# Performance work log

Hardware: AMD Instinct MI355X
Metric: run time of the kernel (lower is better)

Reference implementation:

```python
import jax, jax.numpy as jnp
import numpy as np

B, L, C, H = 8, 1024, 1024, 16  # batch, seq_len, n_embed, n_head


def setup_inputs() -> dict:
    key = jax.random.key(0)
    k0, k1, k2 = jax.random.split(key, 3)
    s = 0.02  # init scale
    return {
        "x": jax.random.normal(k0, (B, L, C), jnp.float32),
        "W_qkv": jax.random.normal(k1, (C, 3 * C), jnp.float32) * s,  # (in, out) layout
        "b_qkv": jnp.zeros((3 * C,), jnp.float32),
        "W_proj": jax.random.normal(k2, (C, C), jnp.float32) * s,
        "b_proj": jnp.zeros((C,), jnp.float32),
    }


def reference(x, W_qkv, b_qkv, W_proj, b_proj):
    Bb, Ll, Cc = x.shape
    d = Cc // H  # head dim
    qkv = x @ W_qkv + b_qkv                      # (B, L, 3C)
    q, k, v = jnp.split(qkv, 3, axis=2)
    q = q.reshape(Bb, Ll, H, d).transpose(0, 2, 1, 3)  # (B, H, L, d)
    k = k.reshape(Bb, Ll, H, d).transpose(0, 2, 1, 3)
    v = v.reshape(Bb, Ll, H, d).transpose(0, 2, 1, 3)
    scale = 1.0 / np.sqrt(d).astype(np.float32)
    attn = jnp.einsum("bhid,bhjd->bhij", q, k) * scale  # (B, H, Lq, Lk)
    causal = jnp.tril(jnp.ones((Ll, Ll), dtype=bool))    # (Lq, Lk)
    attn = jnp.where(causal[None, None, :, :], attn, -jnp.inf)
    # NOTE: source uses F.softmax(attn, dim=2) -> softmax over the QUERY axis.
    attn = jax.nn.softmax(attn, axis=2)
    y = jnp.einsum("bhij,bhjd->bhid", attn, v)           # (B, H, L, d)
    y = y.transpose(0, 2, 1, 3).reshape(Bb, Ll, Cc)      # (B, L, C)
    return y @ W_proj + b_proj
```

## Files before the change

kernel.cpp:

```cpp
#include <hip/hip_runtime.h>

typedef unsigned short u16;
typedef unsigned int   u32;
using bf16x8 = __attribute__((ext_vector_type(8))) short;
using f32x4  = __attribute__((ext_vector_type(4))) float;
using f32x16 = __attribute__((ext_vector_type(16))) float;
using u32x4  = __attribute__((ext_vector_type(4))) u32;

static constexpr int Bb = 8, Ll = 1024, Cc = 1024, Hh = 16, Dd = 64;
static constexpr int Mrows = Bb * Ll;
static constexpr int N3    = 3 * Cc;
static constexpr float QSCALE = 0.125f * 1.44269504088896f;

__device__ __forceinline__ u16 f2b(float f) {
    u32 u = __builtin_bit_cast(u32, f);
    u += 0x7FFFu + ((u >> 16) & 1u);
    return (u16)(u >> 16);
}
__device__ __forceinline__ float b2f(u16 u) {
    return __builtin_bit_cast(float, (u32)u << 16);
}
__device__ __forceinline__ u32 pack2bf(float a, float b) {
    return (u32)f2b(a) | ((u32)f2b(b) << 16);
}
__device__ __forceinline__ void gload16(const u16* g, u16* l) {
    __builtin_amdgcn_global_load_lds(
        (const __attribute__((address_space(1))) void*)g,
        (__attribute__((address_space(3))) void*)l, 16, 0, 0);
}

__global__ void k_prep(const float* __restrict__ x, u16* __restrict__ xb,
                       const float* __restrict__ Wqkv, u16* __restrict__ WqkvT,
                       const float* __restrict__ Wproj, u16* __restrict__ WprojT)
{
    __shared__ float tile[32][33];
    int bid = blockIdx.x;
    int tid = threadIdx.x;
    if (bid < 2048) {
        int idx = bid * 256 + tid;
        #pragma unroll
        for (int h = 0; h < 2; ++h) {
            f32x4 v0 = *((const f32x4*)x + idx * 4 + h * 2);
            f32x4 v1 = *((const f32x4*)x + idx * 4 + h * 2 + 1);
            u32x4 o;
            o[0] = pack2bf(v0[0], v0[1]);
            o[1] = pack2bf(v0[2], v0[3]);
            o[2] = pack2bf(v1[0], v1[1]);
            o[3] = pack2bf(v1[2], v1[3]);
            *((u32x4*)xb + idx * 2 + h) = o;
        }
        return;
    }
    int bz = bid - 2048;
    int bx = bz & 127;
    int by = bz >> 7;
    const float* in; u16* out; int Cn;
    if (bx < 96) { in = Wqkv;  out = WqkvT;  Cn = N3; }
    else         { in = Wproj; out = WprojT; Cn = Cc; bx -= 96; }
    const int R = Cc;
    int tx = tid & 31, ty = tid >> 5;
    int c = bx * 32 + tx;
    int rbase = by * 32;
    #pragma unroll
    for (int rr = 0; rr < 4; ++rr)
        tile[ty + rr * 8][tx] = in[(size_t)(rbase + ty + rr * 8) * Cn + c];
    __syncthreads();
    int ro = bx * 32 + ty;
    #pragma unroll
    for (int rr = 0; rr < 4; ++rr)
        out[(size_t)(ro + rr * 8) * R + rbase + tx] = f2b(tile[tx][ty + rr * 8]);
}

__global__ __launch_bounds__(256, 2)
void k_gemm_qkv32(const u16* __restrict__ A, const u16* __restrict__ Bt,
                  const float* __restrict__ bias,
                  u16* __restrict__ qo, u16* __restrict__ ko, u16* __restrict__ vo)
{
    const int K = Cc;
    const int NT = K / 64;
    __shared__ u16 As[2][128 * 64];
    __shared__ u16 Bs[2][128 * 64];
    const int tid = threadIdx.x;
    const int wid = tid >> 6, lane = tid & 63;
    const int l31 = lane & 31, lhi = lane >> 5, l7 = lane & 7;
    const int wr = wid >> 1, wc = wid & 1;
    const int nwg = gridDim.x * gridDim.y;
    const int flat = blockIdx.y * gridDim.x + blockIdx.x;
    const int swz = (flat & 7) * (nwg >> 3) + (flat >> 3);
    const int bx = swz % gridDim.x, by = swz / gridDim.x;
    const int row0 = by * 128, col0 = bx * 128;

    const int srow = tid >> 3;
    const int schunk = (tid & 7) ^ (srow & 7);
    const u16* gA = A  + (size_t)(row0 + srow) * K + schunk * 8;
    const u16* gB = Bt + (size_t)(col0 + srow) * K + schunk * 8;

#define STG(buf, t) do { \
    const u16* ga_ = gA + (size_t)(t) * 64; \
    const u16* gb_ = gB + (size_t)(t) * 64; \
    u16* la_ = &As[buf][wid * 512]; \
    u16* lb_ = &Bs[buf][wid * 512]; \
    gload16(ga_,                  la_); \
    gload16(ga_ + (size_t)32 * K, la_ + 2048); \
    gload16(ga_ + (size_t)64 * K, la_ + 4096); \
    gload16(ga_ + (size_t)96 * K, la_ + 6144); \
    gload16(gb_,                  lb_); \
    gload16(gb_ + (size_t)32 * K, lb_ + 2048); \
    gload16(gb_ + (size_t)64 * K, lb_ + 4096); \
    gload16(gb_ + (size_t)96 * K, lb_ + 6144); \
} while (0)

    const int coff0 = (((0 + lhi) ^ l7) << 3);
    const int coff1 = (((2 + lhi) ^ l7) << 3);
    const int coff2 = (((4 + lhi) ^ l7) << 3);
    const int coff3 = (((6 + lhi) ^ l7) << 3);
    const int coff[4] = { coff0, coff1, coff2, coff3 };

    f32x16 acc[2][2] = {};

    STG(0, 0);
    STG(1, 1);
    asm volatile("s_waitcnt vmcnt(8)" ::: "memory");
    __builtin_amdgcn_s_barrier();
    __builtin_amdgcn_sched_barrier(0);

    for (int t = 0; t < NT; ++t) {
        const u16* cA = &As[t & 1][0];
        const u16* cB = &Bs[t & 1][0];
        bf16x8 af[2][4], bf0[4];
        #pragma unroll
        for (int tm = 0; tm < 2; ++tm)
            #pragma unroll
            for (int kc = 0; kc < 4; ++kc)
                af[tm][kc] = *(const bf16x8*)&cA[(wr * 64 + tm * 32 + l31) * 64 + coff[kc]];
        #pragma unroll
        for (int kc = 0; kc < 4; ++kc)
            bf0[kc] = *(const bf16x8*)&cB[(wc * 64 + l31) * 64 + coff[kc]];
        __builtin_amdgcn_s_setprio(1);
        #pragma unroll
        for (int tm = 0; tm < 2; ++tm)
            #pragma unroll
            for (int kc = 0; kc < 4; ++kc)
                acc[tm][0] = __builtin_amdgcn_mfma_f32_32x32x16_bf16(
                    af[tm][kc], bf0[kc], acc[tm][0], 0, 0, 0);
        __builtin_amdgcn_s_setprio(0);
        __builtin_amdgcn_s_barrier();
        bf16x8 bf1[4];
        #pragma unroll
        for (int kc = 0; kc < 4; ++kc)
            bf1[kc] = *(const bf16x8*)&cB[(wc * 64 + 32 + l31) * 64 + coff[kc]];
        __builtin_amdgcn_s_setprio(1);
        #pragma unroll
        for (int tm = 0; tm < 2; ++tm)
            #pragma unroll
            for (int kc = 0; kc < 4; ++kc)
                acc[tm][1] = __builtin_amdgcn_mfma_f32_32x32x16_bf16(
                    af[tm][kc], bf1[kc], acc[tm][1], 0, 0, 0);
        __builtin_amdgcn_s_setprio(0);
        __builtin_amdgcn_s_barrier();
        __builtin_amdgcn_sched_barrier(0);
        if (t + 2 < NT) STG(t & 1, t + 2);
        if (t + 1 < NT) {
            if (t + 2 < NT) { asm volatile("s_waitcnt vmcnt(8)" ::: "memory"); }
            else            { asm volatile("s_waitcnt vmcnt(0)" ::: "memory"); }
            __builtin_amdgcn_s_barrier();
            __builtin_amdgcn_sched_barrier(0);
        }
    }
#undef STG

    #pragma unroll
    for (int tm = 0; tm < 2; ++tm) {
        #pragma unroll
        for (int tn = 0; tn < 2; ++tn) {
            int cg = col0 + wc * 64 + tn * 32 + l31;
            float bv = bias[cg];
            int which = cg >> 10;
            float sc = (which == 0) ? QSCALE : 1.0f;
            int cc2 = cg & 1023;
            int h = cc2 >> 6, dd = cc2 & 63;
            int rbase = row0 + wr * 64 + tm * 32 + 4 * lhi;
            #pragma unroll
            for (int g = 0; g < 4; ++g) {
                #pragma unroll
                for (int r = 0; r < 4; ++r) {
                    int rg = rbase + 8 * g + r;
                    int bidx = rg >> 10, ll2 = rg & 1023;
                    size_t o = ((size_t)(bidx * Hh + h) * Ll + ll2) * Dd + dd;
                    u16 val = f2b((acc[tm][tn][g * 4 + r] + bv) * sc);
                    if (which == 0) qo[o] = val;
                    else if (which == 1) ko[o] = val;
                    else vo[o] = val;
                }
            }
        }
    }
}

__global__ __launch_bounds__(256, 2)
void k_gemm_proj32(const u16* __restrict__ A, const u16* __restrict__ Bt,
                   const float* __restrict__ bias, float* __restrict__ outf)
{
    const int K = Cc;
    const int N = Cc;
    const int NT = K / 64;
    __shared__ u16 As[2][128 * 64];
    __shared__ u16 Bs[2][128 * 64];
    const int tid = threadIdx.x;
    const int wid = tid >> 6, lane = tid & 63;
    const int l31 = lane & 31, lhi = lane >> 5, l7 = lane & 7;
    const int wr = wid >> 1, wc = wid & 1;
    const int nwg = gridDim.x * gridDim.y;
    const int flat = blockIdx.y * gridDim.x + blockIdx.x;
    const int swz = (flat & 7) * (nwg >> 3) + (flat >> 3);
    const int bx = swz % gridDim.x, by = swz / gridDim.x;
    const int row0 = by * 128, col0 = bx * 128;

    const int srow = tid >> 3;
    const int schunk = (tid & 7) ^ (srow & 7);
    const u16* gA = A  + (size_t)(row0 + srow) * K + schunk * 8;
    const u16* gB = Bt + (size_t)(col0 + srow) * K + schunk * 8;

#define STG(buf, t) do { \
    const u16* ga_ = gA + (size_t)(t) * 64; \
    const u16* gb_ = gB + (size_t)(t) * 64; \
    u16* la_ = &As[buf][wid * 512]; \
    u16* lb_ = &Bs[buf][wid * 512]; \
    gload16(ga_,                  la_); \
    gload16(ga_ + (size_t)32 * K, la_ + 2048); \
    gload16(ga_ + (size_t)64 * K, la_ + 4096); \
    gload16(ga_ + (size_t)96 * K, la_ + 6144); \
    gload16(gb_,                  lb_); \
    gload16(gb_ + (size_t)32 * K, lb_ + 2048); \
    gload16(gb_ + (size_t)64 * K, lb_ + 4096); \
    gload16(gb_ + (size_t)96 * K, lb_ + 6144); \
} while (0)

    const int coff0 = (((0 + lhi) ^ l7) << 3);
    const int coff1 = (((2 + lhi) ^ l7) << 3);
    const int coff2 = (((4 + lhi) ^ l7) << 3);
    const int coff3 = (((6 + lhi) ^ l7) << 3);
    const int coff[4] = { coff0, coff1, coff2, coff3 };

    f32x16 acc[2][2] = {};

    STG(0, 0);
    STG(1, 1);
    asm volatile("s_waitcnt vmcnt(8)" ::: "memory");
    __builtin_amdgcn_s_barrier();
    __builtin_amdgcn_sched_barrier(0);

    for (int t = 0; t < NT; ++t) {
        const u16* cA = &As[t & 1][0];
        const u16* cB = &Bs[t & 1][0];
        bf16x8 af[2][4], bf0[4];
        #pragma unroll
        for (int tm = 0; tm < 2; ++tm)
            #pragma unroll
            for (int kc = 0; kc < 4; ++kc)
                af[tm][kc] = *(const bf16x8*)&cA[(wr * 64 + tm * 32 + l31) * 64 + coff[kc]];
        #pragma unroll
        for (int kc = 0; kc < 4; ++kc)
            bf0[kc] = *(const bf16x8*)&cB[(wc * 64 + l31) * 64 + coff[kc]];
        __builtin_amdgcn_s_setprio(1);
        #pragma unroll
        for (int tm = 0; tm < 2; ++tm)
            #pragma unroll
            for (int kc = 0; kc < 4; ++kc)
                acc[tm][0] = __builtin_amdgcn_mfma_f32_32x32x16_bf16(
                    af[tm][kc], bf0[kc], acc[tm][0], 0, 0, 0);
        __builtin_amdgcn_s_setprio(0);
        __builtin_amdgcn_s_barrier();
        bf16x8 bf1[4];
        #pragma unroll
        for (int kc = 0; kc < 4; ++kc)
            bf1[kc] = *(const bf16x8*)&cB[(wc * 64 + 32 + l31) * 64 + coff[kc]];
        __builtin_amdgcn_s_setprio(1);
        #pragma unroll
        for (int tm = 0; tm < 2; ++tm)
            #pragma unroll
            for (int kc = 0; kc < 4; ++kc)
                acc[tm][1] = __builtin_amdgcn_mfma_f32_32x32x16_bf16(
                    af[tm][kc], bf1[kc], acc[tm][1], 0, 0, 0);
        __builtin_amdgcn_s_setprio(0);
        __builtin_amdgcn_s_barrier();
        __builtin_amdgcn_sched_barrier(0);
        if (t + 2 < NT) STG(t & 1, t + 2);
        if (t + 1 < NT) {
            if (t + 2 < NT) { asm volatile("s_waitcnt vmcnt(8)" ::: "memory"); }
            else            { asm volatile("s_waitcnt vmcnt(0)" ::: "memory"); }
            __builtin_amdgcn_s_barrier();
            __builtin_amdgcn_sched_barrier(0);
        }
    }
#undef STG

    #pragma unroll
    for (int tm = 0; tm < 2; ++tm) {
        #pragma unroll
        for (int tn = 0; tn < 2; ++tn) {
            int cg = col0 + wc * 64 + tn * 32 + l31;
            float bv = bias[cg];
            int rbase = row0 + wr * 64 + tm * 32 + 4 * lhi;
            #pragma unroll
            for (int g = 0; g < 4; ++g) {
                #pragma unroll
                for (int r = 0; r < 4; ++r) {
                    int rg = rbase + 8 * g + r;
                    outf[(size_t)rg * N + cg] = acc[tm][tn][g * 4 + r] + bv;
                }
            }
        }
    }
}

__global__ __launch_bounds__(256, 4)
void k_attn_colsum_vt(const u16* __restrict__ Q, const u16* __restrict__ Kb,
                      const u16* __restrict__ V, u16* __restrict__ vt)
{
    __shared__ u16 Qs[2][64 * 64];
    __shared__ float zlds[2][64];
    const int tid = threadIdx.x;
    const int wid = tid >> 6, lane = tid & 63;
    const int lr = lane & 15, lg = lane >> 4;
    const int l7 = lr & 7;
    const int fid = blockIdx.x;
    const int xcd = fid & 7, n = fid >> 3;
    const int xtA = n & 7;
    const int xtB = 15 - xtA;
    const int bh = (xcd << 4) | (n >> 3);
    const u16* Qp = Q  + (size_t)bh * Ll * Dd;
    const u16* Kp = Kb + (size_t)bh * Ll * Dd;
    const int jwA = xtA * 64 + wid * 16;
    const int jwB = xtB * 64 + wid * 16;
    bf16x8 kbA0 = *(const bf16x8*)&Kp[(jwA + lr) * Dd + lg * 8];
    bf16x8 kbA1 = *(const bf16x8*)&Kp[(jwA + lr) * Dd + 32 + lg * 8];
    bf16x8 kbB0 = *(const bf16x8*)&Kp[(jwB + lr) * Dd + lg * 8];
    bf16x8 kbB1 = *(const bf16x8*)&Kp[(jwB + lr) * Dd + 32 + lg * 8];
    const bool dmask[4] = { lg * 4 + 0 >= lr, lg * 4 + 1 >= lr,
                            lg * 4 + 2 >= lr, lg * 4 + 3 >= lr };
    const int ch0 = ((lg ^ l7) << 3);
    const int ch1 = (((4 + lg) ^ l7) << 3);
    const int srow = tid >> 3;
    const int schunk = (tid & 7) ^ (srow & 7);
    float zA = 0.f, zB = 0.f;

    const int nA = 16 - xtA;
    const int NS = 17;
#define IOF(s) (((s) < nA) ? (xtA * 64 + 64 * (s)) : (xtB * 64 + 64 * ((s) - nA)))

#define STGQ(buf, I0) do { \
    const u16* g_ = Qp + (size_t)((I0) + srow) * 64 + schunk * 8; \
    u16* l_ = &Qs[buf][wid * 512]; \
    gload16(g_,                   l_); \
    gload16(g_ + (size_t)32 * 64, l_ + 2048); \
} while (0)

#define CS_STEP(buf, I0, JW, KB0, KB1, ZACC) do { \
    const u16* Qs_ = &Qs[buf][0]; \
    _Pragma("unroll") \
    for (int ss = 0; ss < 4; ++ss) { \
        int ib = (I0) + ss * 16; \
        if (ib >= (JW)) { \
            bf16x8 qa0 = *(const bf16x8*)&Qs_[(ss * 16 + lr) * 64 + ch0]; \
            bf16x8 qa1 = *(const bf16x8*)&Qs_[(ss * 16 + lr) * 64 + ch1]; \
            f32x4 s_ = {0.f, 0.f, 0.f, 0.f}; \
            s_ = __builtin_amdgcn_mfma_f32_16x16x32_bf16(qa0, KB0, s_, 0, 0, 0); \
            s_ = __builtin_amdgcn_mfma_f32_16x16x32_bf16(qa1, KB1, s_, 0, 0, 0); \
            if (ib >= (JW) + 16) { \
                _Pragma("unroll") \
                for (int r = 0; r < 4; ++r) ZACC += exp2f(s_[r]); \
            } else { \
                _Pragma("unroll") \
                for (int r = 0; r < 4; ++r) ZACC += dmask[r] ? exp2f(s_[r]) : 0.f; \
            } \
        } \
    } \
} while (0)

    STGQ(0, IOF(0));
    STGQ(1, IOF(1));
    asm volatile("s_waitcnt vmcnt(2)" ::: "memory");
    __builtin_amdgcn_s_barrier();
    __builtin_amdgcn_sched_barrier(0);

    for (int s = 0; s < NS; ++s) {
        if (s < nA) { CS_STEP((s & 1), xtA * 64 + 64 * s, jwA, kbA0, kbA1, zA); }
        else        { CS_STEP((s & 1), xtB * 64 + 64 * (s - nA), jwB, kbB0, kbB1, zB); }
        __builtin_amdgcn_s_barrier();
        __builtin_amdgcn_sched_barrier(0);
        if (s + 2 < NS) STGQ((s & 1), IOF(s + 2));
        if (s + 1 < NS) {
            if (s + 2 < NS) { asm volatile("s_waitcnt vmcnt(2)" ::: "memory"); }
            else            { asm volatile("s_waitcnt vmcnt(0)" ::: "memory"); }
            __builtin_amdgcn_s_barrier();
            __builtin_amdgcn_sched_barrier(0);
        }
    }
#undef STGQ
#undef CS_STEP
#undef IOF

    zA += __shfl_xor(zA, 16); zA += __shfl_xor(zA, 32);
    zB += __shfl_xor(zB, 16); zB += __shfl_xor(zB, 32);
    if (lg == 0) {
        zlds[0][wid * 16 + lr] = 1.f / zA;
        zlds[1][wid * 16 + lr] = 1.f / zB;
    }

    u16* sc = &Qs[0][0];
    const u16* Vr = V + (size_t)bh * Ll * Dd;
    const int lrow = tid >> 2;
    const int seg  = (tid & 3) << 4;
    #pragma unroll
    for (int t = 0; t < 2; ++t) {
        const int jw0 = (t ? xtB : xtA) * 64;
        u32x4 h0 = *(const u32x4*)&Vr[(size_t)(jw0 + lrow) * Dd + seg];
        u32x4 h1 = *(const u32x4*)&Vr[(size_t)(jw0 + lrow) * Dd + seg + 8];
        __syncthreads();
        *(u32x4*)&sc[lrow * 72 + seg]     = h0;
        *(u32x4*)&sc[lrow * 72 + seg + 8] = h1;
        __syncthreads();
        u16 obuf[16];
        #pragma unroll
        for (int j = 0; j < 16; ++j) {
            float zv = zlds[t][seg + j];
            obuf[j] = f2b(b2f(sc[(seg + j) * 72 + lrow]) * zv);
        }
        u16* dst = vt + ((size_t)bh * Dd + lrow) * Ll + jw0 + seg;
        *(u32x4*)dst       = *(u32x4*)&obuf[0];
        *(u32x4*)(dst + 8) = *(u32x4*)&obuf[8];
    }
}

__global__ __launch_bounds__(256, 4)
void k_attn_pv(const u16* __restrict__ Q, const u16* __restrict__ Kb,
               const u16* __restrict__ Vt, u16* __restrict__ Y)
{
    __shared__ u16 Ks[2][64 * 64];
    __shared__ u16 Vs[2][64 * 64];
    const int tid = threadIdx.x;
    const int wid = tid >> 6, lane = tid & 63;
    const int lr = lane & 15, lg = lane >> 4;
    const int l7 = lr & 7;
    const int fid = blockIdx.x;
    const int xcd = fid & 7, n = fid >> 3;
    const int xtA = n & 7;
    const int xtB = 15 - xtA;
    const int bh = (xcd << 4) | (n >> 3);
    const int bidx = bh >> 4, h = bh & 15;
    const u16* Qp = Q  + (size_t)bh * Ll * Dd;
    const u16* Kp = Kb + (size_t)bh * Ll * Dd;
    const u16* Vp = Vt + (size_t)bh * Ll * Dd;
    const int src0 = lr + 32 * (lg & 1);
    const int src1 = src0 + 16;
    const bool selHi = (lg & 2) != 0;
    const int ch0 = ((lg ^ l7) << 3);
    const int ch1 = (((4 + lg) ^ l7) << 3);
    const int srow = tid >> 3;
    const int schunk = (tid & 7) ^ (srow & 7);

    const int iwA = xtA * 64 + wid * 16;
    const int iwB = xtB * 64 + wid * 16;
    bf16x8 qaA0 = *(const bf16x8*)&Qp[(iwA + lr) * Dd + lg * 8];
    bf16x8 qaA1 = *(const bf16x8*)&Qp[(iwA + lr) * Dd + 32 + lg * 8];
    bf16x8 qaB0 = *(const bf16x8*)&Qp[(iwB + lr) * Dd + lg * 8];
    bf16x8 qaB1 = *(const bf16x8*)&Qp[(iwB + lr) * Dd + 32 + lg * 8];
    f32x4 yaccA[4] = {};
    f32x4 yaccB[4] = {};

    const int NS = 17;
#define JOF(s) (((s) <= xtA) ? 64 * (s) : 64 * ((s) - xtA - 1))

#define STGKV(buf, J) do { \
    const u16* gk_ = Kp + (size_t)((J) + srow) * 64 + schunk * 8; \
    const u16* gv_ = Vp + (size_t)srow * Ll + (J) + schunk * 8; \
    u16* lk_ = &Ks[buf][wid * 512]; \
    u16* lv_ = &Vs[buf][wid * 512]; \
    gload16(gk_,                   lk_); \
    gload16(gk_ + (size_t)32 * 64, lk_ + 2048); \
    gload16(gv_,                   lv_); \
    gload16(gv_ + (size_t)32 * Ll, lv_ + 2048); \
} while (0)

#define PV_STEP(buf, J0, IW, QA0, QA1, YACC) do { \
    const u16* Ks_ = &Ks[buf][0]; \
    const u16* Vs_ = &Vs[buf][0]; \
    uint2 w0, w1, w2, w3; \
    _Pragma("unroll") \
    for (int cs = 0; cs < 4; ++cs) { \
        bf16x8 kb0 = *(const bf16x8*)&Ks_[(cs * 16 + lr) * 64 + ch0]; \
        bf16x8 kb1 = *(const bf16x8*)&Ks_[(cs * 16 + lr) * 64 + ch1]; \
        f32x4 s_ = {0.f, 0.f, 0.f, 0.f}; \
        s_ = __builtin_amdgcn_mfma_f32_16x16x32_bf16(kb0, QA0, s_, 0, 0, 0); \
        s_ = __builtin_amdgcn_mfma_f32_16x16x32_bf16(kb1, QA1, s_, 0, 0, 0); \
        int jb = (J0) + cs * 16; \
        float p[4]; \
        if (jb + 15 <= (IW)) { \
            _Pragma("unroll") \
            for (int r = 0; r < 4; ++r) p[r] = exp2f(s_[r]); \
        } else { \
            int ig = (IW) + lr; \
            _Pragma("unroll") \
            for (int r = 0; r < 4; ++r) \
                p[r] = (jb + 4 * lg + r <= ig) ? exp2f(s_[r]) : 0.f; \
        } \
        uint2 w_; \
        w_.x = pack2bf(p[0], p[1]); \
        w_.y = pack2bf(p[2], p[3]); \
        if (cs == 0) w0 = w_; else if (cs == 1) w1 = w_; \
        else if (cs == 2) w2 = w_; else w3 = w_; \
    } \
    u32 a00 = (u32)__shfl((int)w0.x, src0), a01 = (u32)__shfl((int)w0.y, src0); \
    u32 a02 = (u32)__shfl((int)w0.x, src1), a03 = (u32)__shfl((int)w0.y, src1); \
    u32 a10 = (u32)__shfl((int)w1.x, src0), a11 = (u32)__shfl((int)w1.y, src0); \
    u32 a12 = (u32)__shfl((int)w1.x, src1), a13 = (u32)__shfl((int)w1.y, src1); \
    u32 a20 = (u32)__shfl((int)w2.x, src0), a21 = (u32)__shfl((int)w2.y, src0); \
    u32 a22 = (u32)__shfl((int)w2.x, src1), a23 = (u32)__shfl((int)w2.y, src1); \
    u32 a30 = (u32)__shfl((int)w3.x, src0), a31 = (u32)__shfl((int)w3.y, src0); \
    u32 a32 = (u32)__shfl((int)w3.x, src1), a33 = (u32)__shfl((int)w3.y, src1); \
    u32x4 pa0u, pa1u; \
    pa0u[0] = selHi ? a10 : a00;  pa0u[1] = selHi ? a11 : a01; \
    pa0u[2] = selHi ? a12 : a02;  pa0u[3] = selHi ? a13 : a03; \
    pa1u[0] = selHi ? a30 : a20;  pa1u[1] = selHi ? a31 : a21; \
    pa1u[2] = selHi ? a32 : a22;  pa1u[3] = selHi ? a33 : a23; \
    bf16x8 pa0 = __builtin_bit_cast(bf16x8, pa0u); \
    bf16x8 pa1 = __builtin_bit_cast(bf16x8, pa1u); \
    _Pragma("unroll") \
    for (int ns = 0; ns < 4; ++ns) { \
        bf16x8 vb0 = *(const bf16x8*)&Vs_[(ns * 16 + lr) * 64 + ch0]; \
        bf16x8 vb1 = *(const bf16x8*)&Vs_[(ns * 16 + lr) * 64 + ch1]; \
        YACC[ns] = __builtin_amdgcn_mfma_f32_16x16x32_bf16(pa0, vb0, YACC[ns], 0, 0, 0); \
        YACC[ns] = __builtin_amdgcn_mfma_f32_16x16x32_bf16(pa1, vb1, YACC[ns], 0, 0, 0); \
    } \
} while (0)

    STGKV(0, 0);
    STGKV(1, JOF(1));
    asm volatile("s_waitcnt vmcnt(4)" ::: "memory");
    __builtin_amdgcn_s_barrier();
    __builtin_amdgcn_sched_barrier(0);

    for (int s = 0; s < NS; ++s) {
        if (s <= xtA) { PV_STEP((s & 1), 64 * s, iwA, qaA0, qaA1, yaccA); }
        else          { PV_STEP((s & 1), 64 * (s - xtA - 1), iwB, qaB0, qaB1, yaccB); }
        __builtin_amdgcn_s_barrier();
        __builtin_amdgcn_sched_barrier(0);
        if (s + 2 < NS) STGKV((s & 1), JOF(s + 2));
        if (s + 1 < NS) {
            if (s + 2 < NS) { asm volatile("s_waitcnt vmcnt(4)" ::: "memory"); }
            else            { asm volatile("s_waitcnt vmcnt(0)" ::: "memory"); }
            __builtin_amdgcn_s_barrier();
            __builtin_amdgcn_sched_barrier(0);
        }
    }
#undef STGKV
#undef PV_STEP
#undef JOF

    #pragma unroll
    for (int ns = 0; ns < 4; ++ns)
        #pragma unroll
        for (int r = 0; r < 4; ++r) {
            int l2 = iwA + lg * 4 + r;
            Y[((size_t)bidx * Ll + l2) * Cc + h * Dd + ns * 16 + lr] = f2b(yaccA[ns][r]);
        }
    #pragma unroll
    for (int ns = 0; ns < 4; ++ns)
        #pragma unroll
        for (int r = 0; r < 4; ++r) {
            int l2 = iwB + lg * 4 + r;
            Y[((size_t)bidx * Ll + l2) * Cc + h * Dd + ns * 16 + lr] = f2b(yaccB[ns][r]);
        }
}

extern "C" void kernel_launch(void* const* d_in, const int* in_sizes, int n_in,
                              void* d_out, int out_size, void* d_ws, size_t ws_size,
                              hipStream_t stream)
{
    const float* x     = (const float*)d_in[0];
    const float* Wqkv  = (const float*)d_in[1];
    const float* bqkv  = (const float*)d_in[2];
    const float* Wproj = (const float*)d_in[3];
    const float* bproj = (const float*)d_in[4];
    float* out = (float*)d_out;

    char* ws = (char*)d_ws;
    u16* xb     = (u16*)(ws + 0);
    u16* WqkvT  = (u16*)(ws + 16777216);
    u16* WprojT = (u16*)(ws + 23068672);
    u16* q      = (u16*)(ws + 25165824);
    u16* k      = (u16*)(ws + 41943040);
    u16* v      = (u16*)(ws + 58720256);
    u16* vt     = (u16*)(ws + 75497472);

    k_prep<<<dim3(2048 + 4096), dim3(256), 0, stream>>>(x, xb, Wqkv, WqkvT, Wproj, WprojT);
    k_gemm_qkv32<<<dim3(N3 / 128, Mrows / 128), dim3(256), 0, stream>>>(
        xb, WqkvT, bqkv, q, k, v);
    k_attn_colsum_vt<<<dim3(1024), dim3(256), 0, stream>>>(q, k, v, vt);
    k_attn_pv<<<dim3(1024), dim3(256), 0, stream>>>(q, k, vt, v);
    k_gemm_proj32<<<dim3(Cc / 128, Mrows / 128), dim3(256), 0, stream>>>(
        v, WprojT, bproj, out);
}
```

Measured before the change: 175.0 us.

## Use 8 waves per block in QKV GEMM with 64x32 per-wave tiles

Doubles the QKV GEMM block from 256 to 512 threads and regrids the waves as 2x4, each computing 64x32 instead of 64x64. Global-to-LDS staging is split across the extra threads, so each thread issues half as many loads and the vmcnt waits are halved. The second half-step of B-fragment loads and its mid-iteration barrier are removed. The aim is more waves for latency hiding and lower per-wave register pressure, at the cost of more LDS reads per MFMA, since each wave reuses its A fragments over a narrower N slice.

```diff
diff --git a/kernel.cpp b/kernel.cpp
--- a/kernel.cpp
+++ b/kernel.cpp
@@ -71,7 +71,7 @@
         out[(size_t)(ro + rr * 8) * R + rbase + tx] = f2b(tile[tx][ty + rr * 8]);
 }
 
-__global__ __launch_bounds__(256, 2)
+__global__ __launch_bounds__(512, 2)
 void k_gemm_qkv32(const u16* __restrict__ A, const u16* __restrict__ Bt,
                   const float* __restrict__ bias,
                   u16* __restrict__ qo, u16* __restrict__ ko, u16* __restrict__ vo)
@@ -83,7 +83,7 @@
     const int tid = threadIdx.x;
     const int wid = tid >> 6, lane = tid & 63;
     const int l31 = lane & 31, lhi = lane >> 5, l7 = lane & 7;
-    const int wr = wid >> 1, wc = wid & 1;
+    const int wr = wid >> 2, wcn = wid & 3;
     const int nwg = gridDim.x * gridDim.y;
     const int flat = blockIdx.y * gridDim.x + blockIdx.x;
     const int swz = (flat & 7) * (nwg >> 3) + (flat >> 3);
@@ -101,13 +101,9 @@
     u16* la_ = &As[buf][wid * 512]; \
     u16* lb_ = &Bs[buf][wid * 512]; \
     gload16(ga_,                  la_); \
-    gload16(ga_ + (size_t)32 * K, la_ + 2048); \
     gload16(ga_ + (size_t)64 * K, la_ + 4096); \
-    gload16(ga_ + (size_t)96 * K, la_ + 6144); \
     gload16(gb_,                  lb_); \
-    gload16(gb_ + (size_t)32 * K, lb_ + 2048); \
     gload16(gb_ + (size_t)64 * K, lb_ + 4096); \
-    gload16(gb_ + (size_t)96 * K, lb_ + 6144); \
 } while (0)
 
     const int coff0 = (((0 + lhi) ^ l7) << 3);
@@ -116,18 +112,18 @@
     const int coff3 = (((6 + lhi) ^ l7) << 3);
     const int coff[4] = { coff0, coff1, coff2, coff3 };
 
-    f32x16 acc[2][2] = {};
+    f32x16 acc[2] = {};
 
     STG(0, 0);
     STG(1, 1);
-    asm volatile("s_waitcnt vmcnt(8)" ::: "memory");
+    asm volatile("s_waitcnt vmcnt(4)" ::: "memory");
     __builtin_amdgcn_s_barrier();
     __builtin_amdgcn_sched_barrier(0);
 
     for (int t = 0; t < NT; ++t) {
         const u16* cA = &As[t & 1][0];
         const u16* cB = &Bs[t & 1][0];
-        bf16x8 af[2][4], bf0[4];
+        bf16x8 af[2][4], bfv[4];
         #pragma unroll
         for (int tm = 0; tm < 2; ++tm)
             #pragma unroll
@@ -135,33 +131,20 @@
                 af[tm][kc] = *(const bf16x8*)&cA[(wr * 64 + tm * 32 + l31) * 64 + coff[kc]];
         #pragma unroll
         for (int kc = 0; kc < 4; ++kc)
-            bf0[kc] = *(const bf16x8*)&cB[(wc * 64 + l31) * 64 + coff[kc]];
+            bfv[kc] = *(const bf16x8*)&cB[(wcn * 32 + l31) * 64 + coff[kc]];
         __builtin_amdgcn_s_setprio(1);
         #pragma unroll
         for (int tm = 0; tm < 2; ++tm)
             #pragma unroll
             for (int kc = 0; kc < 4; ++kc)
-                acc[tm][0] = __builtin_amdgcn_mfma_f32_32x32x16_bf16(
-                    af[tm][kc], bf0[kc], acc[tm][0], 0, 0, 0);
-        __builtin_amdgcn_s_setprio(0);
-        __builtin_amdgcn_s_barrier();
-        bf16x8 bf1[4];
-        #pragma unroll
-        for (int kc = 0; kc < 4; ++kc)
-            bf1[kc] = *(const bf16x8*)&cB[(wc * 64 + 32 + l31) * 64 + coff[kc]];
-        __builtin_amdgcn_s_setprio(1);
-        #pragma unroll
-        for (int tm = 0; tm < 2; ++tm)
-            #pragma unroll
-            for (int kc = 0; kc < 4; ++kc)
-                acc[tm][1] = __builtin_amdgcn_mfma_f32_32x32x16_bf16(
-                    af[tm][kc], bf1[kc], acc[tm][1], 0, 0, 0);
+                acc[tm] = __builtin_amdgcn_mfma_f32_32x32x16_bf16(
+                    af[tm][kc], bfv[kc], acc[tm], 0, 0, 0);
         __builtin_amdgcn_s_setprio(0);
         __builtin_amdgcn_s_barrier();
         __builtin_amdgcn_sched_barrier(0);
         if (t + 2 < NT) STG(t & 1, t + 2);
         if (t + 1 < NT) {
-            if (t + 2 < NT) { asm volatile("s_waitcnt vmcnt(8)" ::: "memory"); }
+            if (t + 2 < NT) { asm volatile("s_waitcnt vmcnt(4)" ::: "memory"); }
             else            { asm volatile("s_waitcnt vmcnt(0)" ::: "memory"); }
             __builtin_amdgcn_s_barrier();
             __builtin_amdgcn_sched_barrier(0);
@@ -171,27 +154,24 @@
 
     #pragma unroll
     for (int tm = 0; tm < 2; ++tm) {
-        #pragma unroll
-        for (int tn = 0; tn < 2; ++tn) {
-            int cg = col0 + wc * 64 + tn * 32 + l31;
-            float bv = bias[cg];
-            int which = cg >> 10;
-            float sc = (which == 0) ? QSCALE : 1.0f;
-            int cc2 = cg & 1023;
-            int h = cc2 >> 6, dd = cc2 & 63;
-            int rbase = row0 + wr * 64 + tm * 32 + 4 * lhi;
-            #pragma unroll
-            for (int g = 0; g < 4; ++g) {
-                #pragma unroll
-                for (int r = 0; r < 4; ++r) {
-                    int rg = rbase + 8 * g + r;
-                    int bidx = rg >> 10, ll2 = rg & 1023;
-                    size_t o = ((size_t)(bidx * Hh + h) * Ll + ll2) * Dd + dd;
-                    u16 val = f2b((acc[tm][tn][g * 4 + r] + bv) * sc);
-                    if (which == 0) qo[o] = val;
-                    else if (which == 1) ko[o] = val;
-                    else vo[o] = val;
-                }
+        int cg = col0 + wcn * 32 + l31;
+        float bv = bias[cg];
+        int which = cg >> 10;
+        float sc = (which == 0) ? QSCALE : 1.0f;
+        int cc2 = cg & 1023;
+        int h = cc2 >> 6, dd = cc2 & 63;
+        int rbase = row0 + wr * 64 + tm * 32 + 4 * lhi;
+        #pragma unroll
+        for (int g = 0; g < 4; ++g) {
+            #pragma unroll
+            for (int r = 0; r < 4; ++r) {
+                int rg = rbase + 8 * g + r;
+                int bidx = rg >> 10, ll2 = rg & 1023;
+                size_t o = ((size_t)(bidx * Hh + h) * Ll + ll2) * Dd + dd;
+                u16 val = f2b((acc[tm][g * 4 + r] + bv) * sc);
+                if (which == 0) qo[o] = val;
+                else if (which == 1) ko[o] = val;
+                else vo[o] = val;
             }
         }
     }
@@ -595,7 +575,7 @@
     u16* vt     = (u16*)(ws + 75497472);
 
     k_prep<<<dim3(2048 + 4096), dim3(256), 0, stream>>>(x, xb, Wqkv, WqkvT, Wproj, WprojT);
-    k_gemm_qkv32<<<dim3(N3 / 128, Mrows / 128), dim3(256), 0, stream>>>(
+    k_gemm_qkv32<<<dim3(N3 / 128, Mrows / 128), dim3(512), 0, stream>>>(
         xb, WqkvT, bqkv, q, k, v);
     k_attn_colsum_vt<<<dim3(1024), dim3(256), 0, stream>>>(q, k, v, vt);
     k_attn_pv<<<dim3(1024), dim3(256), 0, stream>>>(q, k, vt, v);
```

After: 177.9 us. No clear change (+1.7%).
